# Kernel optimization log

Measured on AMD Instinct MI355X. Metric: run time of the kernel, lower is better.

The kernel has to match this reference:

```python
import jax, jax.numpy as jnp
import numpy as np


def _conv2d(x, w):
    # x: [B,Cin,H,W], w: [Cout,Cin,kh,kw], stride 1, SAME padding
    return jax.lax.conv_general_dilated(x, w, (1, 1), 'SAME',
                                        dimension_numbers=('NCHW', 'OIHW', 'NCHW'))


def _conv1d(x, w):
    # x: [B,Cin,L], w: [Cout,Cin,k], stride 1, SAME padding
    return jax.lax.conv_general_dilated(x, w, (1,), 'SAME',
                                        dimension_numbers=('NCH', 'OIH', 'NCH'))


def setup_inputs() -> dict:
    key = jax.random.key(0)
    ks = jax.random.split(key, 5)
    B, cin, cout, H, W = 8, 256, 256, 64, 64
    x = jax.random.normal(ks[0], (B, cin, H, W), dtype=jnp.float32)
    # Conv weights, small init ~ 1/sqrt(fan_in)
    w_qkv = jax.random.normal(ks[1], (3 * cout, cin, 3, 3), dtype=jnp.float32) * (1.0 / np.sqrt(cin * 9))
    w_mod = jax.random.normal(ks[2], (2 * cout, cout, 3), dtype=jnp.float32) * (1.0 / np.sqrt(cout * 3))
    w_res = jax.random.normal(ks[3], (cout, cin, 1, 1), dtype=jnp.float32) * (1.0 / np.sqrt(cin))
    w_gate = jax.random.normal(ks[4], (cout, cin + cout, 1, 1), dtype=jnp.float32) * (1.0 / np.sqrt(cin + cout))
    return {'x': x, 'w_qkv': w_qkv, 'w_mod': w_mod, 'w_res': w_res, 'w_gate': w_gate}


def reference(x, w_qkv, w_mod, w_res, w_gate):
    B, C, H, W = x.shape
    cout = w_res.shape[0]
    L = H * W
    # qkv projection, then split and flatten spatial dims
    qkv = _conv2d(x, w_qkv).reshape(B, 3, cout, L)  # [B,3,cout,L]
    q, k, v = qkv[:, 0], qkv[:, 1], qkv[:, 2]       # each [B,cout,L]
    # modulation from v along the spatial axis (Conv1d)
    mod = _conv1d(v, w_mod).reshape(B, 2, cout, L)
    qm, km = mod[:, 0], mod[:, 1]
    # negate-relu softmax modulated scores over spatial axis
    m_q = jax.nn.softmax(-jax.nn.relu(q * qm), axis=-1)  # [B,cout,L]
    m_k = jax.nn.softmax(-jax.nn.relu(k * km), axis=-1)  # [B,cout,L]
    scale = 1.0 / jnp.sqrt(jnp.asarray(C, dtype=x.dtype))
    m_attn = jax.nn.softmax(jnp.einsum('bcl,bdl->bcd', m_q, m_k) * scale, axis=-1)  # [B,cout,cout]
    y = jnp.einsum('bcd,bdl->bcl', m_attn, v).reshape(B, cout, H, W)
    # sigmoid-gated residual blend
    g = jax.nn.sigmoid(_conv2d(jnp.concatenate([y, x], axis=1), w_gate))
    return g * _conv2d(x, w_res) + (1.0 - g) * y
```

## Files before the change

### kernel.cpp

```cpp
#include <hip/hip_runtime.h>
#include <cstdint>

typedef unsigned short u16;
using bf16x8 = __attribute__((ext_vector_type(8))) short;
using f32x4  = __attribute__((ext_vector_type(4))) float;

struct alignas(16) V16 { uint32_t a, b, c, d; };
struct alignas(8)  U16x4 { u16 a, b, c, d; };
struct alignas(16) F4 { float x, y, z, w; };

__device__ __forceinline__ u16 f2bf(float f) {
  uint32_t u = __float_as_uint(f);
  u += 0x7fffu + ((u >> 16) & 1u);
  return (u16)(u >> 16);
}
__device__ __forceinline__ float bf2f(u16 h) {
  return __uint_as_float(((uint32_t)h) << 16);
}

#define GLOAD16(g, l) __builtin_amdgcn_global_load_lds(                         \
    (const __attribute__((address_space(1))) uint32_t*)(g),                     \
    (__attribute__((address_space(3))) uint32_t*)(l), 16, 0, 0)

template<int MODE, int MF, int FUSE = 0>
__global__ __launch_bounds__(512, 2) void gemmOv_bf16(
    const u16* __restrict__ A, const u16* __restrict__ B, u16* __restrict__ otr,
    int sA, int sB, int64_t bBatch, int trStride, int64_t trBatch, int MT,
    const u16* __restrict__ zpage,
    const u16* __restrict__ fq = nullptr, u16* __restrict__ eOut = nullptr,
    float* __restrict__ partS = nullptr)
{
  constexpr int NS = (MODE == 2) ? 36 : 12;
  constexpr int ASL = MF * 2048;
  constexpr int SLAB = ASL + 16384;
  __shared__ __align__(16) u16 lds[2 * SLAB];

  const int tid = threadIdx.x;
  const int q = gridDim.x >> 3;
  const int flat = (blockIdx.x & 7) * q + (blockIdx.x >> 3);
  const int per_b = MT * 16;
  const int b = flat / per_b, rem = flat % per_b;
  const int ntile = rem / MT, mtile = rem % MT;
  const int m0 = mtile * (MF * 32), n0 = ntile * 256;
  const u16* Bb = B + (int64_t)b * bBatch;

  const int lane = tid & 63, wave = tid >> 6;
  const int wm = wave >> 2, wn = wave & 3;
  const int lr = lane & 15, lc = lane >> 4;

  const int lrow8 = lane >> 3;
  const int sch  = lane & 7;
  const int scs  = sch ^ (lrow8 & 7);
  const u16* aSrc[MF / 2];
  const u16* bSrc[4];
  int bRow[4];
#pragma unroll
  for (int j = 0; j < MF / 2; ++j)
    aSrc[j] = A + (int64_t)(m0 + wave * (MF * 4) + j * 8 + lrow8) * sA + scs * 8;
#pragma unroll
  for (int j = 0; j < 4; ++j) {
    bRow[j] = n0 + wave * 32 + j * 8 + lrow8;
    bSrc[j] = Bb + (int64_t)bRow[j] * sB + scs * 8;
  }

  auto stageA = [&](int s) {
    const int kOff = (s >> 2) * 256 + ((s & 3) << 6);
    u16* dst = lds + (s & 1) * SLAB + wave * (MF / 2) * 512;
#pragma unroll
    for (int j = 0; j < MF / 2; ++j)
      GLOAD16(aSrc[j] + kOff, dst + j * 512);
  };
  auto stageB = [&](int s) {
    const int tap = s >> 2, kc = (s & 3) << 6;
    int off, dh = 0, dw = 0;
    if constexpr (MODE == 2) { dh = tap / 3 - 1; dw = tap % 3 - 1; off = dh * 64 + dw; }
    else                     { off = tap - 1; }
    u16* dst = lds + (s & 1) * SLAB + ASL + wave * 2048;
#pragma unroll
    for (int j = 0; j < 4; ++j) {
      bool ok;
      if constexpr (MODE == 2) {
        int hh = (bRow[j] >> 6) + dh, ww = (bRow[j] & 63) + dw;
        ok = ((unsigned)hh < 64u) && ((unsigned)ww < 64u);
      } else {
        ok = ((unsigned)(bRow[j] + off) < 4096u);
      }
      const u16* src = ok ? (bSrc[j] + (int64_t)off * sB + kc) : zpage;
      GLOAD16(src, dst + j * 512);
    }
  };

  f32x4 acc[MF][4];
#pragma unroll
  for (int i = 0; i < MF; ++i)
#pragma unroll
    for (int j = 0; j < 4; ++j) acc[i][j] = f32x4{0.f, 0.f, 0.f, 0.f};

  stageA(0); stageB(0);
  asm volatile("s_waitcnt vmcnt(0)" ::: "memory");
  __builtin_amdgcn_s_barrier();
  __builtin_amdgcn_sched_barrier(0);

  for (int s = 0; s < NS; ++s) {
    const u16* As = lds + (s & 1) * SLAB;
    const u16* Bs = As + ASL;
    const bool pf = (s + 1 < NS);
    bf16x8 bfr[4], af[MF];

#pragma unroll
    for (int nf = 0; nf < 4; ++nf) {
      int row = wn * 64 + nf * 16 + lr;
      bfr[nf] = *(const bf16x8*)&Bs[row * 64 + ((lc ^ (row & 7)) * 8)];
    }
#pragma unroll
    for (int mf = 0; mf < MF; ++mf) {
      int row = wm * (MF * 16) + mf * 16 + lr;
      af[mf] = *(const bf16x8*)&As[row * 64 + ((lc ^ (row & 7)) * 8)];
    }
    if (pf) stageA(s + 1);
#pragma unroll
    for (int mf = 0; mf < MF; ++mf)
#pragma unroll
      for (int nf = 0; nf < 4; ++nf)
        acc[mf][nf] = __builtin_amdgcn_mfma_f32_16x16x32_bf16(af[mf], bfr[nf], acc[mf][nf], 0, 0, 0);

#pragma unroll
    for (int nf = 0; nf < 4; ++nf) {
      int row = wn * 64 + nf * 16 + lr;
      bfr[nf] = *(const bf16x8*)&Bs[row * 64 + (((4 + lc) ^ (row & 7)) * 8)];
    }
#pragma unroll
    for (int mf = 0; mf < MF; ++mf) {
      int row = wm * (MF * 16) + mf * 16 + lr;
      af[mf] = *(const bf16x8*)&As[row * 64 + (((4 + lc) ^ (row & 7)) * 8)];
    }
    if (pf) stageB(s + 1);
#pragma unroll
    for (int mf = 0; mf < MF; ++mf)
#pragma unroll
      for (int nf = 0; nf < 4; ++nf)
        acc[mf][nf] = __builtin_amdgcn_mfma_f32_16x16x32_bf16(af[mf], bfr[nf], acc[mf][nf], 0, 0, 0);

    if (pf) {
      asm volatile("s_waitcnt vmcnt(0)" ::: "memory");
      __builtin_amdgcn_s_barrier();
      __builtin_amdgcn_sched_barrier(0);
    }
  }

  if constexpr (FUSE) {
    const u16* qk = fq + (int64_t)b * 4096 * 768;
    u16* eb = eOut + (int64_t)b * 512 * 4096;
    float* ps = partS + (int64_t)b * 512 * 64;
#pragma unroll
    for (int mf = 0; mf < MF; ++mf) {
      const int mbase = m0 + wm * (MF * 16) + mf * 16 + lc * 4;
      float sp[4] = {0.f, 0.f, 0.f, 0.f};
#pragma unroll
      for (int nf = 0; nf < 4; ++nf) {
        int n = n0 + wn * 64 + nf * 16 + lr;
        U16x4 qv = *(const U16x4*)(qk + (int64_t)n * 768 + mbase);
        const u16* qp = (const u16*)&qv;
        f32x4 v = acc[mf][nf];
#pragma unroll
        for (int r = 0; r < 4; ++r) {
          float z = bf2f(qp[r]) * v[r];
          float e = __expf(z > 0.f ? -z : 0.f);
          sp[r] += e;
          eb[(int64_t)(mbase + r) * 4096 + n] = f2bf(e);
        }
      }
#pragma unroll
      for (int r = 0; r < 4; ++r) {
        float sv = sp[r];
        sv += __shfl_xor(sv, 1);
        sv += __shfl_xor(sv, 2);
        sv += __shfl_xor(sv, 4);
        sv += __shfl_xor(sv, 8);
        if (lr == 0)
          ps[(int64_t)(mbase + r) * 64 + ntile * 4 + wn] = sv;
      }
    }
  } else {
#pragma unroll
    for (int mf = 0; mf < MF; ++mf)
#pragma unroll
      for (int nf = 0; nf < 4; ++nf) {
        f32x4 v = acc[mf][nf];
        int m = m0 + wm * (MF * 16) + mf * 16 + lc * 4;
        int n = n0 + wn * 64 + nf * 16 + lr;
        U16x4 pk{f2bf(v[0]), f2bf(v[1]), f2bf(v[2]), f2bf(v[3])};
        *(U16x4*)(otr + trBatch * b + (int64_t)n * trStride + m) = pk;
      }
  }
}

template<int MODE, bool WR_RM, bool WR_TR, bool WR_FOUT = false>
__global__ __launch_bounds__(256) void gemm_bf16(
    const u16* __restrict__ A, const u16* __restrict__ B,
    float* __restrict__ orm, u16* __restrict__ otr,
    int Kc, int sA, int64_t aBatch,
    int sB, int64_t bBatch,
    int rmStride, int64_t rmBatch,
    int trStride, int64_t trBatch,
    int nsplit, int kStep, int64_t splitOut,
    const u16* __restrict__ zpage,
    const float* __restrict__ frs, const u16* __restrict__ fyt)
{
  constexpr int NTAPS = (MODE == 2) ? 9 : (MODE == 1 ? 3 : 1);
  __shared__ __align__(16) u16 As[128 * 32];
  __shared__ __align__(16) u16 Bs[128 * 32];

  const int tid = threadIdx.x;
  int b = blockIdx.z, split = 0;
  if (nsplit > 1) { split = b % nsplit; b /= nsplit; }
  const int m0  = blockIdx.y * 128;
  const int n0  = blockIdx.x * 128;
  const int lane = tid & 63, wave = tid >> 6;
  const int wm = wave >> 1, wn = wave & 1;
  const int lr = lane & 15, lc = lane >> 4;

  f32x4 acc[4][4];
#pragma unroll
  for (int i = 0; i < 4; ++i)
#pragma unroll
    for (int j = 0; j < 4; ++j) acc[i][j] = f32x4{0.f, 0.f, 0.f, 0.f};

  const u16* Ab = A + (int64_t)b * aBatch + split * kStep;
  const u16* Bb = B + (int64_t)b * bBatch + split * kStep;

  const int srow = tid >> 2;
  const int sc   = tid & 3;
  const int scs  = sc ^ (srow & 3);

  for (int t = 0; t < NTAPS; ++t) {
    int dh = 0, dw = 0, off = 0;
    if constexpr (MODE == 2) { dh = t / 3 - 1; dw = t % 3 - 1; off = dh * 64 + dw; }
    if constexpr (MODE == 1) { off = t - 1; }

    for (int kc = 0; kc < Kc; kc += 32) {
      const int kA = t * Kc + kc;
#pragma unroll
      for (int it = 0; it < 2; ++it) {
        int row = srow + it * 64;
        GLOAD16(Ab + (int64_t)(m0 + row) * sA + kA + scs * 8,
                &As[wave * 512 + it * 2048]);
      }
#pragma unroll
      for (int it = 0; it < 2; ++it) {
        int row = srow + it * 64;
        int l = n0 + row;
        int gl = l + off;
        bool ok = true;
        if constexpr (MODE == 2) {
          int hh = (l >> 6) + dh, ww = (l & 63) + dw;
          ok = ((unsigned)hh < 64u) && ((unsigned)ww < 64u);
        }
        if constexpr (MODE == 1) { ok = ((unsigned)gl < 4096u); }
        const u16* src = ok ? (Bb + (int64_t)gl * sB + kc + scs * 8) : zpage;
        GLOAD16(src, &Bs[wave * 512 + it * 2048]);
      }
      __syncthreads();

      bf16x8 af[4], bfr[4];
#pragma unroll
      for (int mf = 0; mf < 4; ++mf) {
        int row = wm * 64 + mf * 16 + lr;
        int cs = lc ^ (row & 3);
        af[mf] = *(const bf16x8*)&As[row * 32 + cs * 8];
      }
#pragma unroll
      for (int nf = 0; nf < 4; ++nf) {
        int row = wn * 64 + nf * 16 + lr;
        int cs = lc ^ (row & 3);
        bfr[nf] = *(const bf16x8*)&Bs[row * 32 + cs * 8];
      }
#pragma unroll
      for (int mf = 0; mf < 4; ++mf)
#pragma unroll
        for (int nf = 0; nf < 4; ++nf)
          acc[mf][nf] = __builtin_amdgcn_mfma_f32_16x16x32_bf16(af[mf], bfr[nf], acc[mf][nf], 0, 0, 0);
      __syncthreads();
    }
  }

#pragma unroll
  for (int mf = 0; mf < 4; ++mf) {
#pragma unroll
    for (int nf = 0; nf < 4; ++nf) {
      f32x4 v = acc[mf][nf];
      int m = m0 + wm * 64 + mf * 16 + lc * 4;
      int n = n0 + wn * 64 + nf * 16 + lr;
      if constexpr (WR_FOUT) {
        int64_t off = rmBatch * b + (int64_t)m * rmStride + n;
        float* p = orm + off;
        const float* pr = frs + off;
        U16x4 yv = *(const U16x4*)(fyt + ((int64_t)(b * 4096 + n)) * 512 + m);
        const u16* yp = (const u16*)&yv;
#pragma unroll
        for (int r = 0; r < 4; ++r) {
          float g = 1.f / (1.f + __expf(-v[r]));
          p[(int64_t)r * rmStride] =
              g * pr[(int64_t)r * rmStride] + (1.f - g) * bf2f(yp[r]);
        }
      }
      if constexpr (WR_RM) {
        float* p = orm + splitOut * split + rmBatch * b + (int64_t)m * rmStride + n;
#pragma unroll
        for (int r = 0; r < 4; ++r) p[(int64_t)r * rmStride] = v[r];
      }
      if constexpr (WR_TR) {
        U16x4 pk{f2bf(v[0]), f2bf(v[1]), f2bf(v[2]), f2bf(v[3])};
        *(U16x4*)(otr + trBatch * b + (int64_t)n * trStride + m) = pk;
      }
    }
  }
}

__global__ void k_zero4(uint32_t* __restrict__ p) { p[threadIdx.x] = 0u; }

__global__ void k_conv_wqkv(const float* __restrict__ w, u16* __restrict__ o) {
  int idx = blockIdx.x * 256 + threadIdx.x;
  if (idx >= 768 * 2304) return;
  int oc = idx / 2304, r = idx % 2304;
  int t = r >> 8, ic = r & 255;
  int kh = t / 3, kw = t % 3;
  o[idx] = f2bf(w[((oc * 256 + ic) * 3 + kh) * 3 + kw]);
}
__global__ void k_conv_wmod(const float* __restrict__ w, u16* __restrict__ o) {
  int idx = blockIdx.x * 256 + threadIdx.x;
  if (idx >= 512 * 768) return;
  int oc = idx / 768, r = idx % 768;
  int t = r >> 8, ic = r & 255;
  o[idx] = f2bf(w[(oc * 256 + ic) * 3 + t]);
}
__global__ void k_convert(const float* __restrict__ in, u16* __restrict__ o, int n) {
  int idx = blockIdx.x * 256 + threadIdx.x;
  if (idx < n) o[idx] = f2bf(in[idx]);
}

__global__ __launch_bounds__(256) void k_xT(const float* __restrict__ x, u16* __restrict__ ycat) {
  __shared__ float tile[64 * 68];
  int b = blockIdx.z, c0 = blockIdx.y * 64, l0 = blockIdx.x * 64;
  int t = threadIdx.x;
  int cc = t >> 2, part = t & 3;
  const float* xp = x + ((int64_t)(b * 256 + c0 + cc)) * 4096 + l0 + part * 16;
#pragma unroll
  for (int j = 0; j < 4; ++j) {
    F4 v = *(const F4*)(xp + j * 4);
    float* tp = &tile[cc * 68 + part * 16 + j * 4];
    tp[0] = v.x; tp[1] = v.y; tp[2] = v.z; tp[3] = v.w;
  }
  __syncthreads();
  int l = t >> 2;
  u16* op = ycat + ((int64_t)b * 4096 + l0 + l) * 512 + 256 + c0 + part * 16;
  __align__(16) u16 tmp[16];
#pragma unroll
  for (int j = 0; j < 16; ++j) tmp[j] = f2bf(tile[(part * 16 + j) * 68 + l]);
  *(V16*)(op) = *(V16*)&tmp[0];
  *(V16*)(op + 8) = *(V16*)&tmp[8];
}

__global__ void k_statsB64(const float* __restrict__ part, float* __restrict__ inv) {
  int idx = blockIdx.x * 256 + threadIdx.x;
  float S = 0.f;
#pragma unroll
  for (int s = 0; s < 64; ++s) S += part[(int64_t)idx * 64 + s];
  inv[idx] = 1.0f / S;
}

__global__ __launch_bounds__(256) void k_softmax_attn(
    const float* __restrict__ sc, const float* __restrict__ invS,
    u16* __restrict__ ma, int nsplit, int64_t splitOff) {
  int c = blockIdx.x, b = blockIdx.y;
  int64_t base = ((int64_t)b * 256 + c) * 256;
  int t = threadIdx.x;
  float z = 0.f;
  for (int s = 0; s < nsplit; ++s) z += sc[(int64_t)s * splitOff + base + t];
  float iq = invS[(int64_t)b * 512 + c];
  float ik = invS[(int64_t)b * 512 + 256 + t];
  z *= iq * ik * 0.0625f;
  __shared__ float red[256];
  red[t] = z; __syncthreads();
  for (int s = 128; s > 0; s >>= 1) { if (t < s) red[t] = fmaxf(red[t], red[t + s]); __syncthreads(); }
  float M = red[0]; __syncthreads();
  float p = __expf(z - M);
  red[t] = p; __syncthreads();
  for (int s = 128; s > 0; s >>= 1) { if (t < s) red[t] += red[t + s]; __syncthreads(); }
  ma[base + t] = f2bf(p / red[0]);
}

extern "C" void kernel_launch(void* const* d_in, const int* in_sizes, int n_in,
                              void* d_out, int out_size, void* d_ws, size_t ws_size,
                              hipStream_t stream) {
  (void)in_sizes; (void)n_in; (void)out_size; (void)ws_size;
  const float* x      = (const float*)d_in[0];
  const float* w_qkv  = (const float*)d_in[1];
  const float* w_mod  = (const float*)d_in[2];
  const float* w_res  = (const float*)d_in[3];
  const float* w_gate = (const float*)d_in[4];
  float* out = (float*)d_out;

  char* p = (char*)d_ws;
  auto take = [&](size_t n) { void* r = (void*)p; p += (n + 255) & ~(size_t)255; return r; };
  u16*    zpage  = (u16*)take(256);
  u16*    qkvT   = (u16*)take(50331648);
  u16*    ycatT  = (u16*)take(33554432);
  u16*    eT     = (u16*)take(33554432);
  float*  scores = (float*)take(16777216);
  u16*    mattn  = (u16*)take(1048576);
  float*  partS  = (float*)take(1048576);
  float*  invS   = (float*)take(16384);
  u16*    Wa     = (u16*)take(3538944);
  u16*    Wb     = (u16*)take(786432);
  u16*    Wg     = (u16*)take(262144);
  u16*    Wr     = (u16*)take(131072);
  float*  resb   = (float*)take(33554432);

  k_zero4<<<1, 64, 0, stream>>>((uint32_t*)zpage);
  k_conv_wqkv<<<6912, 256, 0, stream>>>(w_qkv, Wa);
  k_conv_wmod<<<1536, 256, 0, stream>>>(w_mod, Wb);
  k_convert<<<512, 256, 0, stream>>>(w_gate, Wg, 131072);
  k_convert<<<256, 256, 0, stream>>>(w_res, Wr, 65536);
  k_xT<<<dim3(64, 4, 8), 256, 0, stream>>>(x, ycatT);

  gemmOv_bf16<2, 6><<<512, 512, 0, stream>>>(
      Wa, ycatT + 256, qkvT,
      2304, 512, (int64_t)4096 * 512,
      768, (int64_t)4096 * 768, 4, zpage);

  gemmOv_bf16<1, 8, 1><<<256, 512, 0, stream>>>(
      Wb, qkvT + 512, nullptr,
      768, 768, (int64_t)4096 * 768,
      0, 0, 2, zpage,
      qkvT, eT, partS);

  k_statsB64<<<16, 256, 0, stream>>>(partS, invS);

  gemm_bf16<0, true, false><<<dim3(2, 2, 64), 256, 0, stream>>>(
      eT, eT + (int64_t)256 * 4096, scores, nullptr,
      512, 4096, (int64_t)512 * 4096,
      4096, (int64_t)512 * 4096,
      256, (int64_t)256 * 256,
      0, 0,
      8, 512, (int64_t)8 * 256 * 256, zpage, nullptr, nullptr);

  k_softmax_attn<<<dim3(256, 8), 256, 0, stream>>>(
      scores, invS, mattn, 8, (int64_t)8 * 256 * 256);

  gemm_bf16<0, false, true><<<dim3(32, 2, 8), 256, 0, stream>>>(
      mattn, qkvT + 512, nullptr, ycatT,
      256, 256, (int64_t)256 * 256,
      768, (int64_t)4096 * 768,
      0, 0,
      512, (int64_t)4096 * 512,
      1, 0, 0, zpage, nullptr, nullptr);

  gemm_bf16<0, true, false><<<dim3(32, 2, 8), 256, 0, stream>>>(
      Wr, ycatT + 256, resb, nullptr,
      256, 256, 0,
      512, (int64_t)4096 * 512,
      4096, (int64_t)256 * 4096,
      0, 0,
      1, 0, 0, zpage, nullptr, nullptr);

  gemm_bf16<0, false, false, true><<<dim3(32, 2, 8), 256, 0, stream>>>(
      Wg, ycatT, out, nullptr,
      512, 512, 0,
      512, (int64_t)4096 * 512,
      4096, (int64_t)256 * 4096,
      0, 0,
      1, 0, 0, zpage, resb, ycatT);
}
```

Before: 260.8 us.

## Fuse residual 1x1 conv into gate GEMM and merge weight prep kernels

The residual projection GEMM is folded into the gate GEMM as a second accumulator. It reuses the B tiles already staged for the x half of the concatenated input (K>=256), so a separate kernel launch, the fp32 resb round trip and its re-read in the epilogue all go away. The four weight conversion kernels and the zero-page kernel are merged into one launch, which cuts launch overhead. The cost is an extra 8KB of shared memory and 64 more accumulator registers per thread in the gate kernel, which may lower occupancy.

Result: faster. 248.2 us (-4.9%).

```diff
diff --git a/kernel.cpp b/kernel.cpp
--- a/kernel.cpp
+++ b/kernel.cpp
@@ -195,7 +195,7 @@
   }
 }
 
-template<int MODE, bool WR_RM, bool WR_TR, bool WR_FOUT = false>
+template<int MODE, bool WR_RM, bool WR_TR, bool WR_FOUT = false, bool DUAL = false>
 __global__ __launch_bounds__(256) void gemm_bf16(
     const u16* __restrict__ A, const u16* __restrict__ B,
     float* __restrict__ orm, u16* __restrict__ otr,
@@ -205,11 +205,12 @@
     int trStride, int64_t trBatch,
     int nsplit, int kStep, int64_t splitOut,
     const u16* __restrict__ zpage,
-    const float* __restrict__ frs, const u16* __restrict__ fyt)
+    const u16* __restrict__ fyt, const u16* __restrict__ A2)
 {
   constexpr int NTAPS = (MODE == 2) ? 9 : (MODE == 1 ? 3 : 1);
   __shared__ __align__(16) u16 As[128 * 32];
   __shared__ __align__(16) u16 Bs[128 * 32];
+  __shared__ __align__(16) u16 As2[128 * 32];
 
   const int tid = threadIdx.x;
   int b = blockIdx.z, split = 0;
@@ -225,6 +226,13 @@
   for (int i = 0; i < 4; ++i)
 #pragma unroll
     for (int j = 0; j < 4; ++j) acc[i][j] = f32x4{0.f, 0.f, 0.f, 0.f};
+  f32x4 acc2[4][4];
+  if constexpr (DUAL) {
+#pragma unroll
+    for (int i = 0; i < 4; ++i)
+#pragma unroll
+      for (int j = 0; j < 4; ++j) acc2[i][j] = f32x4{0.f, 0.f, 0.f, 0.f};
+  }
 
   const u16* Ab = A + (int64_t)b * aBatch + split * kStep;
   const u16* Bb = B + (int64_t)b * bBatch + split * kStep;
@@ -240,11 +248,22 @@
 
     for (int kc = 0; kc < Kc; kc += 32) {
       const int kA = t * Kc + kc;
+      const bool dualK = DUAL && (kA >= 256);
 #pragma unroll
       for (int it = 0; it < 2; ++it) {
         int row = srow + it * 64;
         GLOAD16(Ab + (int64_t)(m0 + row) * sA + kA + scs * 8,
                 &As[wave * 512 + it * 2048]);
+      }
+      if constexpr (DUAL) {
+        if (dualK) {
+#pragma unroll
+          for (int it = 0; it < 2; ++it) {
+            int row = srow + it * 64;
+            GLOAD16(A2 + (int64_t)(m0 + row) * 256 + (kA - 256) + scs * 8,
+                    &As2[wave * 512 + it * 2048]);
+          }
+        }
       }
 #pragma unroll
       for (int it = 0; it < 2; ++it) {
@@ -280,6 +299,22 @@
 #pragma unroll
         for (int nf = 0; nf < 4; ++nf)
           acc[mf][nf] = __builtin_amdgcn_mfma_f32_16x16x32_bf16(af[mf], bfr[nf], acc[mf][nf], 0, 0, 0);
+      if constexpr (DUAL) {
+        if (dualK) {
+          bf16x8 af2[4];
+#pragma unroll
+          for (int mf = 0; mf < 4; ++mf) {
+            int row = wm * 64 + mf * 16 + lr;
+            int cs = lc ^ (row & 3);
+            af2[mf] = *(const bf16x8*)&As2[row * 32 + cs * 8];
+          }
+#pragma unroll
+          for (int mf = 0; mf < 4; ++mf)
+#pragma unroll
+            for (int nf = 0; nf < 4; ++nf)
+              acc2[mf][nf] = __builtin_amdgcn_mfma_f32_16x16x32_bf16(af2[mf], bfr[nf], acc2[mf][nf], 0, 0, 0);
+        }
+      }
       __syncthreads();
     }
   }
@@ -294,14 +329,13 @@
       if constexpr (WR_FOUT) {
         int64_t off = rmBatch * b + (int64_t)m * rmStride + n;
         float* p = orm + off;
-        const float* pr = frs + off;
+        f32x4 rv = acc2[mf][nf];
         U16x4 yv = *(const U16x4*)(fyt + ((int64_t)(b * 4096 + n)) * 512 + m);
         const u16* yp = (const u16*)&yv;
 #pragma unroll
         for (int r = 0; r < 4; ++r) {
           float g = 1.f / (1.f + __expf(-v[r]));
-          p[(int64_t)r * rmStride] =
-              g * pr[(int64_t)r * rmStride] + (1.f - g) * bf2f(yp[r]);
+          p[(int64_t)r * rmStride] = g * rv[r] + (1.f - g) * bf2f(yp[r]);
         }
       }
       if constexpr (WR_RM) {
@@ -317,26 +351,35 @@
   }
 }
 
-__global__ void k_zero4(uint32_t* __restrict__ p) { p[threadIdx.x] = 0u; }
-
-__global__ void k_conv_wqkv(const float* __restrict__ w, u16* __restrict__ o) {
-  int idx = blockIdx.x * 256 + threadIdx.x;
-  if (idx >= 768 * 2304) return;
-  int oc = idx / 2304, r = idx % 2304;
-  int t = r >> 8, ic = r & 255;
-  int kh = t / 3, kw = t % 3;
-  o[idx] = f2bf(w[((oc * 256 + ic) * 3 + kh) * 3 + kw]);
-}
-__global__ void k_conv_wmod(const float* __restrict__ w, u16* __restrict__ o) {
-  int idx = blockIdx.x * 256 + threadIdx.x;
-  if (idx >= 512 * 768) return;
-  int oc = idx / 768, r = idx % 768;
-  int t = r >> 8, ic = r & 255;
-  o[idx] = f2bf(w[(oc * 256 + ic) * 3 + t]);
-}
-__global__ void k_convert(const float* __restrict__ in, u16* __restrict__ o, int n) {
-  int idx = blockIdx.x * 256 + threadIdx.x;
-  if (idx < n) o[idx] = f2bf(in[idx]);
+__global__ void k_prep(const float* __restrict__ wqkv, const float* __restrict__ wmod,
+                       const float* __restrict__ wgate, const float* __restrict__ wres,
+                       u16* __restrict__ Wa, u16* __restrict__ Wb,
+                       u16* __restrict__ Wg, u16* __restrict__ Wr,
+                       uint32_t* __restrict__ zpage) {
+  int bid = blockIdx.x, t = threadIdx.x;
+  if (bid < 6912) {
+    int idx = bid * 256 + t;
+    if (idx < 768 * 2304) {
+      int oc = idx / 2304, r = idx % 2304;
+      int tap = r >> 8, ic = r & 255;
+      Wa[idx] = f2bf(wqkv[((oc * 256 + ic) * 3 + tap / 3) * 3 + tap % 3]);
+    }
+  } else if (bid < 8448) {
+    int idx = (bid - 6912) * 256 + t;
+    if (idx < 512 * 768) {
+      int oc = idx / 768, r = idx % 768;
+      int tap = r >> 8, ic = r & 255;
+      Wb[idx] = f2bf(wmod[(oc * 256 + ic) * 3 + tap]);
+    }
+  } else if (bid < 8960) {
+    int idx = (bid - 8448) * 256 + t;
+    if (idx < 131072) Wg[idx] = f2bf(wgate[idx]);
+  } else if (bid < 9216) {
+    int idx = (bid - 8960) * 256 + t;
+    if (idx < 65536) Wr[idx] = f2bf(wres[idx]);
+  } else {
+    if (t < 64) zpage[t] = 0u;
+  }
 }
 
 __global__ __launch_bounds__(256) void k_xT(const float* __restrict__ x, u16* __restrict__ ycat) {
@@ -415,13 +458,9 @@
   u16*    Wb     = (u16*)take(786432);
   u16*    Wg     = (u16*)take(262144);
   u16*    Wr     = (u16*)take(131072);
-  float*  resb   = (float*)take(33554432);
-
-  k_zero4<<<1, 64, 0, stream>>>((uint32_t*)zpage);
-  k_conv_wqkv<<<6912, 256, 0, stream>>>(w_qkv, Wa);
-  k_conv_wmod<<<1536, 256, 0, stream>>>(w_mod, Wb);
-  k_convert<<<512, 256, 0, stream>>>(w_gate, Wg, 131072);
-  k_convert<<<256, 256, 0, stream>>>(w_res, Wr, 65536);
+
+  k_prep<<<9217, 256, 0, stream>>>(w_qkv, w_mod, w_gate, w_res,
+                                   Wa, Wb, Wg, Wr, (uint32_t*)zpage);
   k_xT<<<dim3(64, 4, 8), 256, 0, stream>>>(x, ycatT);
 
   gemmOv_bf16<2, 6><<<512, 512, 0, stream>>>(
@@ -456,19 +495,11 @@
       512, (int64_t)4096 * 512,
       1, 0, 0, zpage, nullptr, nullptr);
 
-  gemm_bf16<0, true, false><<<dim3(32, 2, 8), 256, 0, stream>>>(
-      Wr, ycatT + 256, resb, nullptr,
-      256, 256, 0,
-      512, (int64_t)4096 * 512,
-      4096, (int64_t)256 * 4096,
-      0, 0,
-      1, 0, 0, zpage, nullptr, nullptr);
-
-  gemm_bf16<0, false, false, true><<<dim3(32, 2, 8), 256, 0, stream>>>(
+  gemm_bf16<0, false, false, true, true><<<dim3(32, 2, 8), 256, 0, stream>>>(
       Wg, ycatT, out, nullptr,
       512, 512, 0,
       512, (int64_t)4096 * 512,
       4096, (int64_t)256 * 4096,
       0, 0,
-      1, 0, 0, zpage, resb, ycatT);
-}
+      1, 0, 0, zpage, ycatT, Wr);
+}
```
